# Kernel optimization log

Measured on AMD Instinct MI355X. Metric: run time of the kernel, lower is better.

The kernel has to match this reference:

```python
import jax, jax.numpy as jnp
import numpy as np

DS = 32   # self_obs_dim
DO = 32   # obstacle_obs_dim
D = DS + DO
H = 128   # obstacle_hidden_size
B = 512   # batch_size
A = 16    # num_adv_obs = 2 * num_oppo_obs


def _init_linear(key, fan_in, fan_out):
    kw, kb = jax.random.split(key)
    bound = 1.0 / np.sqrt(fan_in)
    w = jax.random.uniform(kw, (fan_in, fan_out), jnp.float32, -bound, bound)
    b = jax.random.uniform(kb, (fan_out,), jnp.float32, -bound, bound)
    return w, b


def setup_inputs() -> dict:
    key = jax.random.key(0)
    ks = jax.random.split(key, 10)
    obs = jax.random.normal(ks[0], (B, DS), jnp.float32)
    latent = jax.random.normal(ks[1], (B, A, DO), jnp.float32)
    hw1, hb1 = _init_linear(ks[2], D, H)
    hw2, hb2 = _init_linear(ks[3], H, D * H)
    vw1, vb1 = _init_linear(ks[4], H, H)
    vw2, vb2 = _init_linear(ks[5], H, H)
    aw1, ab1 = _init_linear(ks[6], 2 * H, H)
    aw2, ab2 = _init_linear(ks[7], H, H)
    aw3, ab3 = _init_linear(ks[8], H, 1)
    return {
        "obs": obs, "obs_intention_latent": latent,
        "hw1": hw1, "hb1": hb1, "hw2": hw2, "hb2": hb2,
        "vw1": vw1, "vb1": vb1, "vw2": vw2, "vb2": vb2,
        "aw1": aw1, "ab1": ab1, "aw2": aw2, "ab2": ab2,
        "aw3": aw3, "ab3": ab3,
        "num_adv_obs": A, "batch_size": B, "num_groups": 1,
    }


def reference(obs, obs_intention_latent, hw1, hb1, hw2, hb2,
              vw1, vb1, vw2, vb2, aw1, ab1, aw2, ab2, aw3, ab3,
              num_adv_obs, batch_size, num_groups):
    relu = jax.nn.relu
    # flatten opponents (batch-major, matches torch .reshape)
    obs_obstacles = obs_intention_latent.reshape(-1, DO)          # [N, DO]
    # torch .repeat(num_adv_obs, 1) tiles the batch dim
    self_rep = jnp.tile(obs[:, :DS], (num_adv_obs, 1))            # [N, DS]
    mlp_input = jnp.concatenate([self_rep, obs_obstacles], axis=1)  # [N, D]
    # hypernet: per-sample weight [N, D, H]
    h = relu(mlp_input @ hw1 + hb1)
    w = relu(h @ hw2 + hb2).reshape(-1, D, H)
    # per-sample vector-matrix product + tanh
    emb = jnp.tanh(jnp.einsum("nd,ndh->nh", mlp_input, w))        # [N, H]
    # neighbor value MLP
    vals = relu(relu(emb @ vw1 + vb1) @ vw2 + vb2)                # [N, H]
    # attention: concat with per-batch mean embedding
    emb_mean = jnp.mean(emb.reshape(batch_size, -1, H), axis=1)   # [B, H]
    mean_rep = jnp.tile(emb_mean, (num_adv_obs, 1))               # [N, H]
    att_in = jnp.concatenate([emb, mean_rep], axis=1)             # [N, 2H]
    scores = relu(relu(att_in @ aw1 + ab1) @ aw2 + ab2) @ aw3 + ab3  # [N, 1]
    att = jax.nn.softmax(scores.reshape(batch_size, -1), axis=1).reshape(-1, 1)
    weighted = (att * vals).reshape(batch_size, -1, H)
    return jnp.sum(weighted, axis=1)                              # [B, H]
```

## Files before the change

kernel.cpp:

```cpp
#include <hip/hip_runtime.h>
#include <hip/hip_bf16.h>
#include <math.h>

#define BATCH 512
#define NADV  16
#define NROWS (BATCH*NADV)
#define DS    32
#define DO    32
#define DIM   64
#define HID   128
#define WCOLS (DIM*HID)
#define LSTR  136
#define PACK_BLOCKS 276

typedef _Float16 half8 __attribute__((ext_vector_type(8)));
typedef float floatx4 __attribute__((ext_vector_type(4)));

__device__ inline void async_ld16(void* lds, const void* g) {
    __builtin_amdgcn_global_load_lds(
        (const __attribute__((address_space(1))) void*)g,
        (__attribute__((address_space(3))) void*)lds, 16, 0, 0);
}

#define XSW(c) ((((c) >> 2) & 7) << 2)

__global__ __launch_bounds__(256)
void k_prep(const float* __restrict__ obs, const float* __restrict__ latent,
            const float* __restrict__ hw1, const float* __restrict__ hb1,
            const float* __restrict__ hw2, const float* __restrict__ vw1,
            const float* __restrict__ vw2, const float* __restrict__ aw1,
            const float* __restrict__ aw2,
            _Float16* __restrict__ hf,
            _Float16* __restrict__ w2p, _Float16* __restrict__ vw1p,
            _Float16* __restrict__ vw2p, _Float16* __restrict__ aw1p,
            _Float16* __restrict__ aw2p) {
    __shared__ __align__(16) float smem[32 * 132];
    int b = blockIdx.x;
    int tid = threadIdx.x;
    if (b < PACK_BLOCKS) {
        const float* src; _Float16* dst; int N, Kt, jb, kt;
        if (b < 256)      { src = hw2; dst = w2p;  N = WCOLS; Kt = 4; jb = b >> 2; kt = b & 3; }
        else if (b < 260) { src = vw1; dst = vw1p; N = HID;   Kt = 4; jb = 0; kt = b - 256; }
        else if (b < 264) { src = vw2; dst = vw2p; N = HID;   Kt = 4; jb = 0; kt = b - 260; }
        else if (b < 272) { src = aw1; dst = aw1p; N = HID;   Kt = 8; jb = 0; kt = b - 264; }
        else              { src = aw2; dst = aw2p; N = HID;   Kt = 4; jb = 0; kt = b - 272; }
        for (int i = tid; i < 32 * 32; i += 256) {
            int r = i >> 5, c4 = (i & 31) * 4;
            *(float4*)&smem[r * 132 + c4] =
                *(const float4*)(src + (size_t)(kt * 32 + r) * N + jb * 128 + c4);
        }
        __syncthreads();
        for (int i = tid; i < 8 * 64; i += 256) {
            int ctl = i >> 6, ln = i & 63;
            int ct = jb * 8 + ctl;
            int rbase = (ln >> 4) * 8, cc = ctl * 16 + (ln & 15);
            half8 v;
#pragma unroll
            for (int e = 0; e < 8; ++e) v[e] = (_Float16)smem[(rbase + e) * 132 + cc];
            *(half8*)(dst + ((size_t)ct * Kt + kt) * 512 + ln * 8) = v;
        }
    } else {
        int n0 = (b - PACK_BLOCKS) * 16;
        int wave = tid >> 6, lane = tid & 63, l15 = lane & 15, quad = lane >> 4;
        half8 af2[2];
        {
            int n = n0 + l15;
            const float* orow = obs + (size_t)(n & (BATCH - 1)) * DS + quad * 8;
            const float* lrow = latent + (size_t)n * DO + quad * 8;
#pragma unroll
            for (int e = 0; e < 8; ++e) {
                af2[0][e] = (_Float16)orow[e];
                af2[1][e] = (_Float16)lrow[e];
            }
        }
#pragma unroll
        for (int cti = 0; cti < 2; ++cti) {
            int ct = wave * 2 + cti;
            float bb = hb1[ct * 16 + l15];
            floatx4 acc = {bb, bb, bb, bb};
#pragma unroll
            for (int ks = 0; ks < 2; ++ks) {
                const float* wsrc = hw1 + (size_t)(ks * 32 + quad * 8) * HID + ct * 16 + l15;
                half8 bf;
#pragma unroll
                for (int e = 0; e < 8; ++e) bf[e] = (_Float16)wsrc[(size_t)e * HID];
                acc = __builtin_amdgcn_mfma_f32_16x16x32_f16(af2[ks], bf, acc, 0, 0, 0);
            }
#pragma unroll
            for (int reg = 0; reg < 4; ++reg)
                hf[(size_t)(n0 + quad * 4 + reg) * HID + ct * 16 + l15] =
                    (_Float16)fmaxf(acc[reg], 0.f);
        }
    }
}

__global__ __launch_bounds__(256, 2)
void k_gemm(const float* __restrict__ obs, const float* __restrict__ latent,
            const _Float16* __restrict__ hf, const _Float16* __restrict__ w2p,
            const float* __restrict__ hb2,
            _Float16* __restrict__ embf, _Float16* __restrict__ emeanf) {
    __shared__ __align__(16) char smraw[81920];
    float (*xs_t)[128] = (float(*)[128])smraw;
    _Float16 (*Bs)[3][2048] = (_Float16(*)[3][2048])(smraw + 32768);

    int b   = blockIdx.x;
    int tid = threadIdx.x;
    int wave = tid >> 6, lane = tid & 63, l15 = lane & 15, quad = lane >> 4;

    int jt = b & 7;
    int rt = b >> 3;
    int n0 = rt * 128;
    int j0 = jt * 16;

    for (int i = tid; i < 128 * 16; i += 256) {
        int r = i >> 4, c4 = (i & 15) * 4;
        float4 v;
        if (c4 < DS) v = *(const float4*)(obs + ((n0 + r) & (BATCH - 1)) * DS + c4);
        else         v = *(const float4*)(latent + (size_t)(n0 + r) * DO + (c4 - DS));
        xs_t[c4 + 0][r ^ XSW(c4 + 0)] = v.x;
        xs_t[c4 + 1][r ^ XSW(c4 + 1)] = v.y;
        xs_t[c4 + 2][r ^ XSW(c4 + 2)] = v.z;
        xs_t[c4 + 3][r ^ XSW(c4 + 3)] = v.w;
    }

    half8 af[8][4];
#pragma unroll
    for (int t = 0; t < 8; ++t)
#pragma unroll
        for (int ks = 0; ks < 4; ++ks)
            af[t][ks] = *(const half8*)(hf + (size_t)(n0 + t * 16 + l15) * HID
                                           + ks * 32 + quad * 8);

    float bias_r[16];
#pragma unroll
    for (int i = 0; i < 16; ++i) {
        int d = (i >> 1) * 8 + wave * 2 + (i & 1);
        bias_r[i] = hb2[d * HID + j0 + l15];
    }

    const _Float16* wbase = w2p + (size_t)jt * 2048 + lane * 8;
#pragma unroll
    for (int p = 0; p < 3; ++p) {
        int d = (p >> 1) * 8 + wave * 2 + (p & 1);
        const _Float16* src = wbase + (size_t)d * 16384;
        _Float16* dst = &Bs[wave][p][0];
#pragma unroll
        for (int kt = 0; kt < 4; ++kt)
            async_ld16(dst + kt * 512, src + kt * 512);
    }
    __syncthreads();

    float emb_acc[8][4];
#pragma unroll
    for (int t = 0; t < 8; ++t)
#pragma unroll
        for (int reg = 0; reg < 4; ++reg) emb_acc[t][reg] = 0.f;

#pragma unroll
    for (int i = 0; i < 16; ++i) {
        if (i <= 13)      asm volatile("s_waitcnt vmcnt(8)" ::: "memory");
        else if (i == 14) asm volatile("s_waitcnt vmcnt(4)" ::: "memory");
        else              asm volatile("s_waitcnt vmcnt(0)" ::: "memory");
        __builtin_amdgcn_sched_barrier(0);

        int d = (i >> 1) * 8 + wave * 2 + (i & 1);
        int buf = i % 3;
        half8 bfr0 = *(const half8*)&Bs[wave][buf][0 * 512 + lane * 8];
        half8 bfr1 = *(const half8*)&Bs[wave][buf][1 * 512 + lane * 8];
        half8 bfr2 = *(const half8*)&Bs[wave][buf][2 * 512 + lane * 8];
        half8 bfr3 = *(const half8*)&Bs[wave][buf][3 * 512 + lane * 8];
        float bb = bias_r[i];
        int rsw = XSW(d);

        __builtin_amdgcn_s_setprio(1);
#pragma unroll
        for (int t = 0; t < 8; ++t) {
            floatx4 acc = {bb, bb, bb, bb};
            acc = __builtin_amdgcn_mfma_f32_16x16x32_f16(af[t][0], bfr0, acc, 0, 0, 0);
            acc = __builtin_amdgcn_mfma_f32_16x16x32_f16(af[t][1], bfr1, acc, 0, 0, 0);
            acc = __builtin_amdgcn_mfma_f32_16x16x32_f16(af[t][2], bfr2, acc, 0, 0, 0);
            acc = __builtin_amdgcn_mfma_f32_16x16x32_f16(af[t][3], bfr3, acc, 0, 0, 0);
            floatx4 xv = *(const floatx4*)&xs_t[d][(t * 16 + quad * 4) ^ rsw];
#pragma unroll
            for (int reg = 0; reg < 4; ++reg)
                emb_acc[t][reg] = fmaf(xv[reg], fmaxf(acc[reg], 0.f), emb_acc[t][reg]);
        }
        __builtin_amdgcn_s_setprio(0);

        if (i + 3 < 16) {
            int dn = ((i + 3) >> 1) * 8 + wave * 2 + ((i + 3) & 1);
            const _Float16* src = wbase + (size_t)dn * 16384;
            _Float16* dst = &Bs[wave][buf][0];
#pragma unroll
            for (int kt = 0; kt < 4; ++kt)
                async_ld16(dst + kt * 512, src + kt * 512);
        }
    }
    __syncthreads();

    float* red = (float*)smraw;
#pragma unroll
    for (int t = 0; t < 8; ++t)
#pragma unroll
        for (int reg = 0; reg < 4; ++reg)
            red[((wave * 128) + t * 16 + quad * 4 + reg) * 16 + l15] = emb_acc[t][reg];
    __syncthreads();
#pragma unroll
    for (int t2 = 0; t2 < 2; ++t2) {
        float e[4];
#pragma unroll
        for (int rr = 0; rr < 4; ++rr) {
            int row = wave * 32 + t2 * 16 + quad * 4 + rr;
            float s = red[(0 * 128 + row) * 16 + l15] + red[(1 * 128 + row) * 16 + l15]
                    + red[(2 * 128 + row) * 16 + l15] + red[(3 * 128 + row) * 16 + l15];
            e[rr] = tanhf(s);
            embf[(size_t)(n0 + row) * HID + j0 + l15] = (_Float16)e[rr];
        }
        float m = e[0] + e[1] + e[2] + e[3];
        m += __shfl_xor(m, 16, 64);
        m += __shfl_xor(m, 32, 64);
        if (quad == 0)
            emeanf[(size_t)(rt * 8 + wave * 2 + t2) * HID + j0 + l15] =
                (_Float16)(m * (1.f / 16));
    }
}

__global__ __launch_bounds__(512, 4)
void k_tail(const _Float16* __restrict__ embf, const _Float16* __restrict__ emeanf,
            const _Float16* __restrict__ vw1p, const float* __restrict__ vb1,
            const _Float16* __restrict__ vw2p, const float* __restrict__ vb2,
            const _Float16* __restrict__ aw1p, const float* __restrict__ ab1,
            const _Float16* __restrict__ aw2p, const float* __restrict__ ab2,
            const float* __restrict__ aw3, const float* __restrict__ ab3,
            float* __restrict__ out) {
    __shared__ _Float16 embs[16][LSTR];
    __shared__ _Float16 means[16][LSTR];
    __shared__ _Float16 tAs[16][LSTR];
    __shared__ _Float16 tBs[16][LSTR];
    __shared__ float scr[16][32];
    __shared__ float satt[16];
    __shared__ float att[16];
    int g = blockIdx.x;
    int n0 = g * 16;
    int tid = threadIdx.x;
    int wave = tid >> 6, lane = tid & 63, l15 = lane & 15, quad = lane >> 4;
    int ct = wave;

    {
        int m = tid >> 8, r = (tid >> 4) & 15, c8 = (tid & 15) * 8;
        if (m == 0)
            *(half8*)&embs[r][c8] = *(const half8*)(embf + (size_t)(n0 + r) * HID + c8);
        else
            *(half8*)&means[r][c8] =
                *(const half8*)(emeanf + (size_t)((n0 & 511) + r) * HID + c8);
    }
    __syncthreads();

    half8 av[4], amean[4];
#pragma unroll
    for (int ks = 0; ks < 4; ++ks) {
        av[ks]    = *(const half8*)&embs[l15][ks * 32 + quad * 8];
        amean[ks] = *(const half8*)&means[l15][ks * 32 + quad * 8];
    }

    floatx4 acc;
    {
        float bb = vb1[ct * 16 + l15];
        acc = (floatx4){bb, bb, bb, bb};
    }
#pragma unroll
    for (int ks = 0; ks < 4; ++ks) {
        half8 bfr = *(const half8*)(vw1p + ((size_t)ct * 4 + ks) * 512 + lane * 8);
        acc = __builtin_amdgcn_mfma_f32_16x16x32_f16(av[ks], bfr, acc, 0, 0, 0);
    }
#pragma unroll
    for (int reg = 0; reg < 4; ++reg)
        tAs[quad * 4 + reg][ct * 16 + l15] = (_Float16)fmaxf(acc[reg], 0.f);
    __syncthreads();

    half8 at[4];
#pragma unroll
    for (int ks = 0; ks < 4; ++ks)
        at[ks] = *(const half8*)&tAs[l15][ks * 32 + quad * 8];

    floatx4 vacc;
    {
        float bb = vb2[ct * 16 + l15];
        vacc = (floatx4){bb, bb, bb, bb};
    }
#pragma unroll
    for (int ks = 0; ks < 4; ++ks) {
        half8 bfr = *(const half8*)(vw2p + ((size_t)ct * 4 + ks) * 512 + lane * 8);
        vacc = __builtin_amdgcn_mfma_f32_16x16x32_f16(at[ks], bfr, vacc, 0, 0, 0);
    }

    floatx4 aacc;
    {
        float bb = ab1[ct * 16 + l15];
        aacc = (floatx4){bb, bb, bb, bb};
    }
#pragma unroll
    for (int ks = 0; ks < 8; ++ks) {
        half8 bfr = *(const half8*)(aw1p + ((size_t)ct * 8 + ks) * 512 + lane * 8);
        half8 a = (ks < 4) ? av[ks] : amean[ks - 4];
        aacc = __builtin_amdgcn_mfma_f32_16x16x32_f16(a, bfr, aacc, 0, 0, 0);
    }
#pragma unroll
    for (int reg = 0; reg < 4; ++reg)
        tBs[quad * 4 + reg][ct * 16 + l15] = (_Float16)fmaxf(aacc[reg], 0.f);
    __syncthreads();

    half8 aa[4];
#pragma unroll
    for (int ks = 0; ks < 4; ++ks)
        aa[ks] = *(const half8*)&tBs[l15][ks * 32 + quad * 8];

    floatx4 a2acc;
    {
        float bb = ab2[ct * 16 + l15];
        a2acc = (floatx4){bb, bb, bb, bb};
    }
#pragma unroll
    for (int ks = 0; ks < 4; ++ks) {
        half8 bfr = *(const half8*)(aw2p + ((size_t)ct * 4 + ks) * 512 + lane * 8);
        a2acc = __builtin_amdgcn_mfma_f32_16x16x32_f16(aa[ks], bfr, a2acc, 0, 0, 0);
    }
    __syncthreads();
#pragma unroll
    for (int reg = 0; reg < 4; ++reg)
        tAs[quad * 4 + reg][ct * 16 + l15] = (_Float16)fmaxf(a2acc[reg], 0.f);
    __syncthreads();

    {
        int r = tid >> 5, ch = tid & 31;
        float p = 0.f;
#pragma unroll
        for (int k = 0; k < 4; ++k)
            p += (float)tAs[r][ch * 4 + k] * aw3[ch * 4 + k];
        scr[r][ch] = p;
    }
    __syncthreads();
    if (tid < 16) {
        float s = ab3[0];
#pragma unroll
        for (int ch = 0; ch < 32; ++ch) s += scr[tid][ch];
        satt[tid] = s;
    }
    __syncthreads();
    if (tid < 16) {
        float m = -1e30f;
#pragma unroll
        for (int a = 0; a < 16; ++a) m = fmaxf(m, satt[a]);
        float S = 0.f;
#pragma unroll
        for (int a = 0; a < 16; ++a) S += expf(satt[a] - m);
        att[tid] = expf(satt[tid] - m) / S;
    }
    __syncthreads();

    {
        float p = 0.f;
#pragma unroll
        for (int reg = 0; reg < 4; ++reg)
            p += att[quad * 4 + reg] * fmaxf(vacc[reg], 0.f);
        p += __shfl_xor(p, 16, 64);
        p += __shfl_xor(p, 32, 64);
        if (quad == 0) out[(size_t)g * HID + ct * 16 + l15] = p;
    }
}

extern "C" void kernel_launch(void* const* d_in, const int* in_sizes, int n_in,
                              void* d_out, int out_size, void* d_ws, size_t ws_size,
                              hipStream_t stream) {
    const float* obs = (const float*)d_in[0];
    const float* lat = (const float*)d_in[1];
    const float* hw1 = (const float*)d_in[2];
    const float* hb1 = (const float*)d_in[3];
    const float* hw2 = (const float*)d_in[4];
    const float* hb2 = (const float*)d_in[5];
    const float* vw1 = (const float*)d_in[6];
    const float* vb1 = (const float*)d_in[7];
    const float* vw2 = (const float*)d_in[8];
    const float* vb2 = (const float*)d_in[9];
    const float* aw1 = (const float*)d_in[10];
    const float* ab1 = (const float*)d_in[11];
    const float* aw2 = (const float*)d_in[12];
    const float* ab2 = (const float*)d_in[13];
    const float* aw3 = (const float*)d_in[14];
    const float* ab3 = (const float*)d_in[15];
    float* out = (float*)d_out;

    char* ws = (char*)d_ws;
    _Float16*  hf     = (_Float16*)ws;  ws += (size_t)NROWS * HID * 2;
    _Float16*  w2p    = (_Float16*)ws;  ws += (size_t)WCOLS * HID * 2;
    _Float16*  embf   = (_Float16*)ws;  ws += (size_t)NROWS * HID * 2;
    _Float16*  emeanf = (_Float16*)ws;  ws += (size_t)BATCH * HID * 2;
    _Float16*  vw1p   = (_Float16*)ws;  ws += (size_t)HID * HID * 2;
    _Float16*  vw2p   = (_Float16*)ws;  ws += (size_t)HID * HID * 2;
    _Float16*  aw1p   = (_Float16*)ws;  ws += (size_t)2 * HID * HID * 2;
    _Float16*  aw2p   = (_Float16*)ws;  ws += (size_t)HID * HID * 2;

    hipLaunchKernelGGL(k_prep, dim3(PACK_BLOCKS + NROWS / 16), dim3(256), 0, stream,
                       obs, lat, hw1, hb1, hw2, vw1, vw2, aw1, aw2,
                       hf, w2p, vw1p, vw2p, aw1p, aw2p);
    hipLaunchKernelGGL(k_gemm, dim3(512), dim3(256), 0, stream,
                       obs, lat, hf, w2p, hb2, embf, emeanf);
    hipLaunchKernelGGL(k_tail, dim3(BATCH), dim3(512), 0, stream,
                       embf, emeanf, vw1p, vb1, vw2p, vb2,
                       aw1p, ab1, aw2p, ab2, aw3, ab3, out);
}
```

Baseline: 132.0 us.

## Shrink gemm row tile to 64 and stream W2 fragments via registers

Halves the row tile of the main hypernet GEMM kernel from 128 to 64, doubling the grid to 1024 blocks. The LDS triple-buffered async global-to-LDS pipeline for W2 is replaced by direct register loads with one-step software prefetch. Each wave now owns 16 contiguous d values instead of an interleaved set. This cuts LDS use and register pressure to raise occupancy, but each block reuses every W2 fragment over half as many rows, so global/L2 traffic for W2 doubles.

```diff
diff --git a/kernel.cpp b/kernel.cpp
--- a/kernel.cpp
+++ b/kernel.cpp
@@ -15,12 +15,6 @@
 
 typedef _Float16 half8 __attribute__((ext_vector_type(8)));
 typedef float floatx4 __attribute__((ext_vector_type(4)));
-
-__device__ inline void async_ld16(void* lds, const void* g) {
-    __builtin_amdgcn_global_load_lds(
-        (const __attribute__((address_space(1))) void*)g,
-        (__attribute__((address_space(3))) void*)lds, 16, 0, 0);
-}
 
 #define XSW(c) ((((c) >> 2) & 7) << 2)
 
@@ -95,13 +89,12 @@
 }
 
 __global__ __launch_bounds__(256, 2)
-void k_gemm(const float* __restrict__ obs, const float* __restrict__ latent,
-            const _Float16* __restrict__ hf, const _Float16* __restrict__ w2p,
-            const float* __restrict__ hb2,
+void k_gemm(const _Float16* __restrict__ hf, const _Float16* __restrict__ w2p,
+            const float* __restrict__ hb2, const float* __restrict__ obs,
+            const float* __restrict__ latent,
             _Float16* __restrict__ embf, _Float16* __restrict__ emeanf) {
-    __shared__ __align__(16) char smraw[81920];
-    float (*xs_t)[128] = (float(*)[128])smraw;
-    _Float16 (*Bs)[3][2048] = (_Float16(*)[3][2048])(smraw + 32768);
+    __shared__ __align__(16) char smraw[16384 + 128];
+    float (*xs_t)[64] = (float(*)[64])smraw;
 
     int b   = blockIdx.x;
     int tid = threadIdx.x;
@@ -109,10 +102,10 @@
 
     int jt = b & 7;
     int rt = b >> 3;
-    int n0 = rt * 128;
+    int n0 = rt * 64;
     int j0 = jt * 16;
 
-    for (int i = tid; i < 128 * 16; i += 256) {
+    for (int i = tid; i < 64 * 16; i += 256) {
         int r = i >> 4, c4 = (i & 15) * 4;
         float4 v;
         if (c4 < DS) v = *(const float4*)(obs + ((n0 + r) & (BATCH - 1)) * DS + c4);
@@ -123,96 +116,72 @@
         xs_t[c4 + 3][r ^ XSW(c4 + 3)] = v.w;
     }
 
-    half8 af[8][4];
-#pragma unroll
-    for (int t = 0; t < 8; ++t)
+    half8 af[4][4];
+#pragma unroll
+    for (int t = 0; t < 4; ++t)
 #pragma unroll
         for (int ks = 0; ks < 4; ++ks)
             af[t][ks] = *(const half8*)(hf + (size_t)(n0 + t * 16 + l15) * HID
                                            + ks * 32 + quad * 8);
-
-    float bias_r[16];
-#pragma unroll
+    __syncthreads();
+
+    float emb_acc[4][4];
+#pragma unroll
+    for (int t = 0; t < 4; ++t)
+#pragma unroll
+        for (int reg = 0; reg < 4; ++reg) emb_acc[t][reg] = 0.f;
+
+    const _Float16* wbase = w2p + (size_t)jt * 2048 + lane * 8;
+    const _Float16* wp = wbase + (size_t)(wave * 16) * 16384;
+    half8 b0 = *(const half8*)(wp + 0 * 512);
+    half8 b1 = *(const half8*)(wp + 1 * 512);
+    half8 b2 = *(const half8*)(wp + 2 * 512);
+    half8 b3 = *(const half8*)(wp + 3 * 512);
+
+#pragma unroll 2
     for (int i = 0; i < 16; ++i) {
-        int d = (i >> 1) * 8 + wave * 2 + (i & 1);
-        bias_r[i] = hb2[d * HID + j0 + l15];
-    }
-
-    const _Float16* wbase = w2p + (size_t)jt * 2048 + lane * 8;
-#pragma unroll
-    for (int p = 0; p < 3; ++p) {
-        int d = (p >> 1) * 8 + wave * 2 + (p & 1);
-        const _Float16* src = wbase + (size_t)d * 16384;
-        _Float16* dst = &Bs[wave][p][0];
-#pragma unroll
-        for (int kt = 0; kt < 4; ++kt)
-            async_ld16(dst + kt * 512, src + kt * 512);
-    }
-    __syncthreads();
-
-    float emb_acc[8][4];
-#pragma unroll
-    for (int t = 0; t < 8; ++t)
-#pragma unroll
-        for (int reg = 0; reg < 4; ++reg) emb_acc[t][reg] = 0.f;
-
-#pragma unroll
-    for (int i = 0; i < 16; ++i) {
-        if (i <= 13)      asm volatile("s_waitcnt vmcnt(8)" ::: "memory");
-        else if (i == 14) asm volatile("s_waitcnt vmcnt(4)" ::: "memory");
-        else              asm volatile("s_waitcnt vmcnt(0)" ::: "memory");
-        __builtin_amdgcn_sched_barrier(0);
-
-        int d = (i >> 1) * 8 + wave * 2 + (i & 1);
-        int buf = i % 3;
-        half8 bfr0 = *(const half8*)&Bs[wave][buf][0 * 512 + lane * 8];
-        half8 bfr1 = *(const half8*)&Bs[wave][buf][1 * 512 + lane * 8];
-        half8 bfr2 = *(const half8*)&Bs[wave][buf][2 * 512 + lane * 8];
-        half8 bfr3 = *(const half8*)&Bs[wave][buf][3 * 512 + lane * 8];
-        float bb = bias_r[i];
+        int d = wave * 16 + i;
+        half8 n0_, n1_, n2_, n3_;
+        if (i < 15) {
+            const _Float16* np = wbase + (size_t)(d + 1) * 16384;
+            n0_ = *(const half8*)(np + 0 * 512);
+            n1_ = *(const half8*)(np + 1 * 512);
+            n2_ = *(const half8*)(np + 2 * 512);
+            n3_ = *(const half8*)(np + 3 * 512);
+        }
+        float bb = hb2[d * HID + j0 + l15];
         int rsw = XSW(d);
-
-        __builtin_amdgcn_s_setprio(1);
-#pragma unroll
-        for (int t = 0; t < 8; ++t) {
+#pragma unroll
+        for (int t = 0; t < 4; ++t) {
             floatx4 acc = {bb, bb, bb, bb};
-            acc = __builtin_amdgcn_mfma_f32_16x16x32_f16(af[t][0], bfr0, acc, 0, 0, 0);
-            acc = __builtin_amdgcn_mfma_f32_16x16x32_f16(af[t][1], bfr1, acc, 0, 0, 0);
-            acc = __builtin_amdgcn_mfma_f32_16x16x32_f16(af[t][2], bfr2, acc, 0, 0, 0);
-            acc = __builtin_amdgcn_mfma_f32_16x16x32_f16(af[t][3], bfr3, acc, 0, 0, 0);
+            acc = __builtin_amdgcn_mfma_f32_16x16x32_f16(af[t][0], b0, acc, 0, 0, 0);
+            acc = __builtin_amdgcn_mfma_f32_16x16x32_f16(af[t][1], b1, acc, 0, 0, 0);
+            acc = __builtin_amdgcn_mfma_f32_16x16x32_f16(af[t][2], b2, acc, 0, 0, 0);
+            acc = __builtin_amdgcn_mfma_f32_16x16x32_f16(af[t][3], b3, acc, 0, 0, 0);
             floatx4 xv = *(const floatx4*)&xs_t[d][(t * 16 + quad * 4) ^ rsw];
 #pragma unroll
             for (int reg = 0; reg < 4; ++reg)
                 emb_acc[t][reg] = fmaf(xv[reg], fmaxf(acc[reg], 0.f), emb_acc[t][reg]);
         }
-        __builtin_amdgcn_s_setprio(0);
-
-        if (i + 3 < 16) {
-            int dn = ((i + 3) >> 1) * 8 + wave * 2 + ((i + 3) & 1);
-            const _Float16* src = wbase + (size_t)dn * 16384;
-            _Float16* dst = &Bs[wave][buf][0];
-#pragma unroll
-            for (int kt = 0; kt < 4; ++kt)
-                async_ld16(dst + kt * 512, src + kt * 512);
-        }
+        b0 = n0_; b1 = n1_; b2 = n2_; b3 = n3_;
     }
     __syncthreads();
 
     float* red = (float*)smraw;
 #pragma unroll
-    for (int t = 0; t < 8; ++t)
+    for (int t = 0; t < 4; ++t)
 #pragma unroll
         for (int reg = 0; reg < 4; ++reg)
-            red[((wave * 128) + t * 16 + quad * 4 + reg) * 16 + l15] = emb_acc[t][reg];
-    __syncthreads();
-#pragma unroll
-    for (int t2 = 0; t2 < 2; ++t2) {
+            red[(wave * 64 + t * 16 + quad * 4 + reg) * 16 + l15] = emb_acc[t][reg];
+    __syncthreads();
+
+    {
         float e[4];
 #pragma unroll
         for (int rr = 0; rr < 4; ++rr) {
-            int row = wave * 32 + t2 * 16 + quad * 4 + rr;
-            float s = red[(0 * 128 + row) * 16 + l15] + red[(1 * 128 + row) * 16 + l15]
-                    + red[(2 * 128 + row) * 16 + l15] + red[(3 * 128 + row) * 16 + l15];
+            int row = wave * 16 + quad * 4 + rr;
+            float s = red[(0 * 64 + row) * 16 + l15] + red[(1 * 64 + row) * 16 + l15]
+                    + red[(2 * 64 + row) * 16 + l15] + red[(3 * 64 + row) * 16 + l15];
             e[rr] = tanhf(s);
             embf[(size_t)(n0 + row) * HID + j0 + l15] = (_Float16)e[rr];
         }
@@ -220,7 +189,7 @@
         m += __shfl_xor(m, 16, 64);
         m += __shfl_xor(m, 32, 64);
         if (quad == 0)
-            emeanf[(size_t)(rt * 8 + wave * 2 + t2) * HID + j0 + l15] =
+            emeanf[(size_t)(rt * 4 + wave) * HID + j0 + l15] =
                 (_Float16)(m * (1.f / 16));
     }
 }
@@ -403,8 +372,8 @@
     hipLaunchKernelGGL(k_prep, dim3(PACK_BLOCKS + NROWS / 16), dim3(256), 0, stream,
                        obs, lat, hw1, hb1, hw2, vw1, vw2, aw1, aw2,
                        hf, w2p, vw1p, vw2p, aw1p, aw2p);
-    hipLaunchKernelGGL(k_gemm, dim3(512), dim3(256), 0, stream,
-                       obs, lat, hf, w2p, hb2, embf, emeanf);
+    hipLaunchKernelGGL(k_gemm, dim3(1024), dim3(256), 0, stream,
+                       hf, w2p, hb2, obs, lat, embf, emeanf);
     hipLaunchKernelGGL(k_tail, dim3(BATCH), dim3(512), 0, stream,
                        embf, emeanf, vw1p, vb1, vw2p, vb2,
                        aw1p, ab1, aw2p, ab2, aw3, ab3, out);
```

Measured after the change: 134.5 us. About the same (+1.9%).
